# Optimization experiments

Measured on AMD Instinct MI355X. Metric: run time of the kernel, lower is better.

## Reference

```python
import jax, jax.numpy as jnp
import numpy as np

B, S, WIDTH, H = 4, 1024, 1024, 16
DH = WIDTH // H
NEG = -1000000000.0


def setup_inputs() -> dict:
    key = jax.random.key(0)
    ks = jax.random.split(key, 11)
    sc = 0.02
    return {
        "inp": jax.random.normal(ks[0], (B, S, WIDTH), dtype=jnp.float32),
        "mask": jax.random.randint(ks[1], (B, 1, S, S), 0, 2, dtype=jnp.int32),
        "wq": jax.random.normal(ks[2], (WIDTH, WIDTH), dtype=jnp.float32) * sc,
        "bq": jax.random.normal(ks[3], (WIDTH,), dtype=jnp.float32) * sc,
        "wk": jax.random.normal(ks[4], (WIDTH, WIDTH), dtype=jnp.float32) * sc,
        "bk": jax.random.normal(ks[5], (WIDTH,), dtype=jnp.float32) * sc,
        "wv": jax.random.normal(ks[6], (WIDTH, WIDTH), dtype=jnp.float32) * sc,
        "bv": jax.random.normal(ks[7], (WIDTH,), dtype=jnp.float32) * sc,
        "wo": jax.random.normal(ks[8], (WIDTH, WIDTH), dtype=jnp.float32) * sc,
        "bo": jax.random.normal(ks[9], (WIDTH,), dtype=jnp.float32) * sc,
    }


def reference(inp, mask, wq, bq, wk, bk, wv, bv, wo, bo):
    # torch Linear: y = x @ W.T + b
    q = inp @ wq.T + bq  # [B,S,WIDTH]
    k = inp @ wk.T + bk
    v = inp @ wv.T + bv
    # split heads -> [B,H,S,DH]
    q = q.reshape(B, S, H, DH).transpose(0, 2, 1, 3)
    k = k.reshape(B, S, H, DH).transpose(0, 2, 1, 3)
    v = v.reshape(B, S, H, DH).transpose(0, 2, 1, 3)
    scale = 1.0 / jnp.sqrt(jnp.float32(DH))
    qk = jnp.einsum("bhqd,bhkd->bhqk", q, k) * scale  # [B,H,S,S]
    qk = jnp.where(mask == 0, jnp.float32(NEG), qk)
    # NOTE: faithful to source, softmax over dim=1 (the HEAD axis), not keys
    attn = jax.nn.softmax(qk, axis=1)
    x = jnp.einsum("bhqk,bhkd->bhqd", attn, v)  # [B,H,S,DH]
    x = x.transpose(0, 2, 1, 3).reshape(B, S, WIDTH)
    return x @ wo.T + bo
```

## Files before the change

### kernel.cpp

```cpp
#include <hip/hip_runtime.h>


typedef float f32x4 __attribute__((ext_vector_type(4)));
typedef __bf16 bf16x8 __attribute__((ext_vector_type(8)));

__device__ __forceinline__ unsigned short f2bf(float f){
  unsigned int u = __builtin_bit_cast(unsigned int, f);
  u = (u + 0x7FFFu + ((u >> 16) & 1u)) >> 16;
  return (unsigned short)u;
}

__device__ __forceinline__ void gl16(const unsigned short* g, unsigned short* l){
  __builtin_amdgcn_global_load_lds(
      (const __attribute__((address_space(1))) void*)g,
      (__attribute__((address_space(3))) void*)l, 16, 0, 0);
}

__global__ __launch_bounds__(256) void cvt_kernel(const float* __restrict__ s,
                                                  unsigned short* __restrict__ d, int n4){
  int i = blockIdx.x * 256 + threadIdx.x;
  if (i < n4){
    float4 v = ((const float4*)s)[i];
    ushort4 o;
    o.x = f2bf(v.x); o.y = f2bf(v.y); o.z = f2bf(v.z); o.w = f2bf(v.w);
    ((ushort4*)d)[i] = o;
  }
}

__global__ __launch_bounds__(256) void cvt4_kernel(
    const float* __restrict__ s0, const float* __restrict__ s1,
    const float* __restrict__ s2, const float* __restrict__ s3,
    unsigned short* __restrict__ d0, unsigned short* __restrict__ d1,
    unsigned short* __restrict__ d2, unsigned short* __restrict__ d3){
  int i = blockIdx.x * 256 + threadIdx.x;
  int seg = i >> 18, j = i & 262143;
  const float* s = (seg == 0) ? s0 : (seg == 1) ? s1 : (seg == 2) ? s2 : s3;
  unsigned short* d = (seg == 0) ? d0 : (seg == 1) ? d1 : (seg == 2) ? d2 : d3;
  float4 v = ((const float4*)s)[j];
  ushort4 o;
  o.x = f2bf(v.x); o.y = f2bf(v.y); o.z = f2bf(v.z); o.w = f2bf(v.w);
  ((ushort4*)d)[j] = o;
}

template<int MODE>
__global__ __launch_bounds__(256) void gemm_bt(
    const unsigned short* __restrict__ A, const unsigned short* __restrict__ Wt,
    int M, int N, int K,
    float* __restrict__ outp,
    unsigned short* __restrict__ qws, unsigned short* __restrict__ kws,
    unsigned short* __restrict__ vws,
    const float* __restrict__ bias0, const float* __restrict__ bias1,
    const float* __restrict__ bias2)
{
  __shared__ unsigned short As_[128*32];
  __shared__ unsigned short Bs_[128*32];
  const int tid = threadIdx.x;
  const int lane = tid & 63;
  const int wid = tid >> 6;
  const int wr = wid >> 1, wc = wid & 1;
  const int m0 = blockIdx.x * 128, n0 = blockIdx.y * 128;
  const int lq = lane & 15, lg = lane >> 4;
  const int srow = (wid << 5) + (lane >> 2);
  const int scol = (lane & 3) << 3;
  const unsigned short* Ag = A  + (size_t)(m0 + srow)*K + scol;
  const unsigned short* Bg = Wt + (size_t)(n0 + srow)*K + scol;
  char* a_l0 = (char*)As_ + (wid << 11);
  char* b_l0 = (char*)Bs_ + (wid << 11);
  f32x4 acc[4][4] = {};

  for (int k0 = 0; k0 < K; k0 += 32){
    gl16(Ag + k0,                 (unsigned short*)a_l0);
    gl16(Ag + (size_t)16*K + k0,  (unsigned short*)(a_l0 + 1024));
    gl16(Bg + k0,                 (unsigned short*)b_l0);
    gl16(Bg + (size_t)16*K + k0,  (unsigned short*)(b_l0 + 1024));
    __syncthreads();
    bf16x8 af[4], wf[4];
    #pragma unroll
    for (int i = 0; i < 4; ++i){
      af[i] = *(const bf16x8*)((char*)As_ + ((((wr<<6)+(i<<4)+lq)) << 6) + (lg << 4));
      wf[i] = *(const bf16x8*)((char*)Bs_ + ((((wc<<6)+(i<<4)+lq)) << 6) + (lg << 4));
    }
    #pragma unroll
    for (int i = 0; i < 4; ++i)
      #pragma unroll
      for (int j = 0; j < 4; ++j)
        acc[i][j] = __builtin_amdgcn_mfma_f32_16x16x32_bf16(af[i], wf[j], acc[i][j], 0, 0, 0);
    __syncthreads();
  }

  if (MODE == 0){
    #pragma unroll
    for (int j = 0; j < 4; ++j){
      int ncol = n0 + wc*64 + j*16 + lq;
      float bv = bias0[ncol];
      #pragma unroll
      for (int i = 0; i < 4; ++i){
        int mrow = m0 + wr*64 + i*16 + lg*4;
        #pragma unroll
        for (int r = 0; r < 4; ++r)
          outp[(size_t)(mrow + r)*N + ncol] = acc[i][j][r] + bv;
      }
    }
  } else {
    const int sel = n0 >> 10;
    const float* bp = (sel == 0) ? bias0 : ((sel == 1) ? bias1 : bias2);
    #pragma unroll
    for (int j = 0; j < 4; ++j){
      int n  = n0 + wc*64 + j*16 + lq;
      int n1 = n & 1023;
      int h = n1 >> 6, d = n1 & 63;
      float bv = bp[n1];
      #pragma unroll
      for (int i = 0; i < 4; ++i){
        int mbase = m0 + wr*64 + i*16 + lg*4;
        #pragma unroll
        for (int r = 0; r < 4; ++r){
          int m = mbase + r;
          int b = m >> 10, s = m & 1023;
          unsigned short o = f2bf(acc[i][j][r] + bv);
          if (sel == 0)      qws[(size_t)((((b<<4) + h)<<10) + s)*64 + d] = o;
          else if (sel == 1) kws[(size_t)((((b<<4) + h)<<10) + s)*64 + d] = o;
          else               vws[(size_t)((((b<<4) + h)<<6) + d)*1024 + s] = o;
        }
      }
    }
  }
}

__global__ __launch_bounds__(512, 4) void qksm_kernel(
    const unsigned short* __restrict__ qws, const unsigned short* __restrict__ kws,
    const int* __restrict__ mask, unsigned short* __restrict__ pws, int qbase)
{
  __shared__ unsigned short Qs[16*16*64];
  const int tid = threadIdx.x;
  const int lane = tid & 63, w = tid >> 6;
  const int kt = blockIdx.x, qt = blockIdx.y, b = blockIdx.z;
  const int q0 = qbase + (qt << 4);
  const int lq = lane & 15, lg = lane >> 4;
  const int aswz = (lq & 7) << 4;

  for (int c = tid; c < 2048; c += 512){
    int e = c << 3;
    int h = e >> 10, q = (e >> 6) & 15, d0 = e & 63;
    uint4 v = *(const uint4*)(qws + (size_t)((((b<<4) + h)<<10) + q0 + q)*64 + d0);
    int byteoff = (((h<<10) + (q<<6) + d0) << 1) ^ ((q & 7) << 4);
    *(uint4*)((char*)Qs + byteoff) = v;
  }
  __syncthreads();

  const float kscale = 0.125f * 1.44269504f;
  for (int it = 0; it < 2; ++it){
    const int kb = (kt << 8) + (it << 7) + (w << 4);
    const int klocal = (it << 7) + (w << 4) + lq;
    f32x4 sc[16];
    #pragma unroll
    for (int h = 0; h < 16; ++h){
      int abase = (h << 11) + (lq << 7) + (lg << 4);
      bf16x8 a0 = *(const bf16x8*)((const char*)Qs + ((abase     ) ^ aswz));
      bf16x8 a1 = *(const bf16x8*)((const char*)Qs + ((abase + 64) ^ aswz));
      const unsigned short* kp = kws + (size_t)((((b<<4) + h)<<10) + kb + lq)*64 + (lg<<3);
      bf16x8 kf0 = *(const bf16x8*)(kp);
      bf16x8 kf1 = *(const bf16x8*)(kp + 32);
      f32x4 s = {};
      s = __builtin_amdgcn_mfma_f32_16x16x32_bf16(a0, kf0, s, 0, 0, 0);
      s = __builtin_amdgcn_mfma_f32_16x16x32_bf16(a1, kf1, s, 0, 0, 0);
      sc[h] = s;
    }
    const int* mp = mask + (size_t)((b<<10) + q0 + (lg<<2))*1024 + kb + lq;
    #pragma unroll
    for (int r = 0; r < 4; ++r){
      const int mv = mp[r << 10];
      float mx = sc[0][r];
      #pragma unroll
      for (int h = 1; h < 16; ++h) mx = fmaxf(mx, sc[h][r]);
      float e[16]; float sum = 0.f;
      #pragma unroll
      for (int h = 0; h < 16; ++h){
        e[h] = __builtin_amdgcn_exp2f((sc[h][r] - mx) * kscale);
        sum += e[h];
      }
      const float rs = __builtin_amdgcn_rcpf(sum);
      const int qloc = (qt << 4) + (lg << 2) + r;
      unsigned short* pp = pws + (b << 23) + (kt << 17) + (qloc << 8) + klocal;
      #pragma unroll
      for (int h = 0; h < 16; ++h){
        float pv = mv ? (e[h] * rs) : 0.0625f;
        pp[h << 19] = f2bf(pv);
      }
    }
  }
}

__global__ __launch_bounds__(256) void pv_kernel(
    const unsigned short* __restrict__ pws, const unsigned short* __restrict__ vws,
    unsigned short* __restrict__ xbf, int qbase)
{
  __shared__ unsigned short Ps_[128*32];
  __shared__ unsigned short Vs_[64*32];
  const int tid = threadIdx.x;
  const int lane = tid & 63;
  const int wid = tid >> 6;
  const int qt = blockIdx.x, bh = blockIdx.y;
  const int b = bh >> 4, h = bh & 15;
  const int lq = lane & 15, lg = lane >> 4;
  const int arow = (wid << 5) + (lane >> 2);
  const int scol = (lane & 3) << 3;
  const unsigned short* Ag = pws + ((size_t)bh << 19) + (((qt << 7) + arow) << 8) + scol;
  const int brow = (wid << 4) + (lane >> 2);
  const unsigned short* Bg = vws + ((size_t)bh << 16) + brow*1024 + scol;
  char* a_l0 = (char*)Ps_ + (wid << 11);
  char* b_l0 = (char*)Vs_ + (wid << 10);
  f32x4 acc[2][4] = {};

  for (int k0 = 0; k0 < 1024; k0 += 32){
    const int koff = ((k0 >> 8) << 17) + (k0 & 255);
    gl16(Ag + koff,              (unsigned short*)a_l0);
    gl16(Ag + koff + (16 << 8),  (unsigned short*)(a_l0 + 1024));
    gl16(Bg + k0,                (unsigned short*)b_l0);
    __syncthreads();
    bf16x8 af[2], wf[4];
    #pragma unroll
    for (int i = 0; i < 2; ++i)
      af[i] = *(const bf16x8*)((char*)Ps_ + ((((wid<<5)+(i<<4)+lq)) << 6) + (lg << 4));
    #pragma unroll
    for (int j = 0; j < 4; ++j)
      wf[j] = *(const bf16x8*)((char*)Vs_ + ((((j<<4)+lq)) << 6) + (lg << 4));
    #pragma unroll
    for (int i = 0; i < 2; ++i)
      #pragma unroll
      for (int j = 0; j < 4; ++j)
        acc[i][j] = __builtin_amdgcn_mfma_f32_16x16x32_bf16(af[i], wf[j], acc[i][j], 0, 0, 0);
    __syncthreads();
  }

  #pragma unroll
  for (int j = 0; j < 4; ++j){
    int d = (j << 4) + lq;
    #pragma unroll
    for (int i = 0; i < 2; ++i){
      #pragma unroll
      for (int r = 0; r < 4; ++r){
        int qrow = qbase + (qt << 7) + (wid << 5) + (i << 4) + (lg << 2) + r;
        xbf[(size_t)((b << 10) + qrow)*1024 + (h << 6) + d] = f2bf(acc[i][j][r]);
      }
    }
  }
}

extern "C" void kernel_launch(void* const* d_in, const int* in_sizes, int n_in,
                              void* d_out, int out_size, void* d_ws, size_t ws_size,
                              hipStream_t stream) {
  const float* inp = (const float*)d_in[0];
  const int*  mask = (const int*)d_in[1];
  const float* wq = (const float*)d_in[2];
  const float* bq = (const float*)d_in[3];
  const float* wk = (const float*)d_in[4];
  const float* bk = (const float*)d_in[5];
  const float* wv = (const float*)d_in[6];
  const float* bv = (const float*)d_in[7];
  const float* wo = (const float*)d_in[8];
  const float* bo = (const float*)d_in[9];
  float* out = (float*)d_out;

  char* ws = (char*)d_ws;
  unsigned short* inp_bf = (unsigned short*)(ws);
  unsigned short* wqkv   = (unsigned short*)(ws + (8u  << 20));
  unsigned short* wo_bf  = (unsigned short*)(ws + (14u << 20));
  unsigned short* qws    = (unsigned short*)(ws + (16u << 20));
  unsigned short* kws    = (unsigned short*)(ws + (24u << 20));
  unsigned short* vws    = (unsigned short*)(ws + (32u << 20));
  unsigned short* xbf    = (unsigned short*)(ws + (40u << 20));
  unsigned short* pws    = (unsigned short*)(ws + (48u << 20));

  cvt_kernel<<<4096, 256, 0, stream>>>(inp, inp_bf, 1048576);
  cvt4_kernel<<<4096, 256, 0, stream>>>(wq, wk, wv, wo,
                                        wqkv, wqkv + (1u << 20), wqkv + (2u << 20), wo_bf);

  gemm_bt<1><<<dim3(32, 24), 256, 0, stream>>>(inp_bf, wqkv, 4096, 3072, 1024,
                                               nullptr, qws, kws, vws, bq, bk, bv);

  for (int half = 0; half < 2; ++half){
    qksm_kernel<<<dim3(4, 32, 4), 512, 0, stream>>>(qws, kws, mask, pws, half * 512);
    pv_kernel<<<dim3(4, 64), 256, 0, stream>>>(pws, vws, xbf, half * 512);
  }

  gemm_bt<0><<<dim3(32, 8), 256, 0, stream>>>(xbf, wo_bf, 4096, 1024, 1024,
                                              out, nullptr, nullptr, nullptr, bo, nullptr, nullptr);
}
```

Baseline: 381.6 us.

## Stage softmax probabilities in LDS for coalesced row-major P stores

The QK-softmax kernel now writes its probabilities to a swizzled LDS tile and then copies them to global memory as 16-byte vector stores. This replaces the old scattered 2-byte stores with a plain row-major [b,h,q,k] layout, and the PV kernel's addressing is updated to match. Q is no longer staged in LDS but read straight from global per head. The change aims to cut uncoalesced write traffic, at the cost of two extra barriers per iteration and more global reads of Q.

```diff
diff --git a/kernel.cpp b/kernel.cpp
--- a/kernel.cpp
+++ b/kernel.cpp
@@ -131,34 +131,24 @@
     const unsigned short* __restrict__ qws, const unsigned short* __restrict__ kws,
     const int* __restrict__ mask, unsigned short* __restrict__ pws, int qbase)
 {
-  __shared__ unsigned short Qs[16*16*64];
+  __shared__ unsigned short Ps[32768];
   const int tid = threadIdx.x;
   const int lane = tid & 63, w = tid >> 6;
   const int kt = blockIdx.x, qt = blockIdx.y, b = blockIdx.z;
   const int q0 = qbase + (qt << 4);
   const int lq = lane & 15, lg = lane >> 4;
-  const int aswz = (lq & 7) << 4;
-
-  for (int c = tid; c < 2048; c += 512){
-    int e = c << 3;
-    int h = e >> 10, q = (e >> 6) & 15, d0 = e & 63;
-    uint4 v = *(const uint4*)(qws + (size_t)((((b<<4) + h)<<10) + q0 + q)*64 + d0);
-    int byteoff = (((h<<10) + (q<<6) + d0) << 1) ^ ((q & 7) << 4);
-    *(uint4*)((char*)Qs + byteoff) = v;
-  }
-  __syncthreads();
-
+  const int buf = w >> 2, ksub = w & 3;
   const float kscale = 0.125f * 1.44269504f;
+
   for (int it = 0; it < 2; ++it){
     const int kb = (kt << 8) + (it << 7) + (w << 4);
-    const int klocal = (it << 7) + (w << 4) + lq;
     f32x4 sc[16];
     #pragma unroll
     for (int h = 0; h < 16; ++h){
-      int abase = (h << 11) + (lq << 7) + (lg << 4);
-      bf16x8 a0 = *(const bf16x8*)((const char*)Qs + ((abase     ) ^ aswz));
-      bf16x8 a1 = *(const bf16x8*)((const char*)Qs + ((abase + 64) ^ aswz));
-      const unsigned short* kp = kws + (size_t)((((b<<4) + h)<<10) + kb + lq)*64 + (lg<<3);
+      const unsigned short* qp = qws + (size_t)((((b<<4)+h)<<10) + q0 + lq)*64 + (lg<<3);
+      bf16x8 a0 = *(const bf16x8*)(qp);
+      bf16x8 a1 = *(const bf16x8*)(qp + 32);
+      const unsigned short* kp = kws + (size_t)((((b<<4)+h)<<10) + kb + lq)*64 + (lg<<3);
       bf16x8 kf0 = *(const bf16x8*)(kp);
       bf16x8 kf1 = *(const bf16x8*)(kp + 32);
       f32x4 s = {};
@@ -180,14 +170,27 @@
         sum += e[h];
       }
       const float rs = __builtin_amdgcn_rcpf(sum);
-      const int qloc = (qt << 4) + (lg << 2) + r;
-      unsigned short* pp = pws + (b << 23) + (kt << 17) + (qloc << 8) + klocal;
+      const int q = (lg << 2) + r;
+      const int base = (buf << 15) | (q << 7) | (((ksub << 4) | lq) << 1);
+      const int swz = lg << 5;
       #pragma unroll
       for (int h = 0; h < 16; ++h){
         float pv = mv ? (e[h] * rs) : 0.0625f;
-        pp[h << 19] = f2bf(pv);
-      }
-    }
+        *(unsigned short*)((char*)Ps + ((base | (h << 11)) ^ swz)) = f2bf(pv);
+      }
+    }
+    __syncthreads();
+    #pragma unroll
+    for (int j = 0; j < 8; ++j){
+      int e = ((j << 9) + tid) << 3;
+      int bufr = e >> 14, h = (e >> 10) & 15, q = (e >> 6) & 15, k64 = e & 63;
+      int lbyte = (e << 1) ^ (((q >> 2) & 3) << 5);
+      uint4 v = *(const uint4*)((const char*)Ps + lbyte);
+      size_t go = ((size_t)b << 23) + ((size_t)h << 19) + ((size_t)((qt << 4) | q) << 10)
+                + (kt << 8) + (it << 7) + (bufr << 6) + k64;
+      *(uint4*)(pws + go) = v;
+    }
+    __syncthreads();
   }
 }
 
@@ -205,7 +208,7 @@
   const int lq = lane & 15, lg = lane >> 4;
   const int arow = (wid << 5) + (lane >> 2);
   const int scol = (lane & 3) << 3;
-  const unsigned short* Ag = pws + ((size_t)bh << 19) + (((qt << 7) + arow) << 8) + scol;
+  const unsigned short* Ag = pws + ((size_t)bh << 19) + ((size_t)((qt << 7) + arow) << 10) + scol;
   const int brow = (wid << 4) + (lane >> 2);
   const unsigned short* Bg = vws + ((size_t)bh << 16) + brow*1024 + scol;
   char* a_l0 = (char*)Ps_ + (wid << 11);
@@ -213,10 +216,9 @@
   f32x4 acc[2][4] = {};
 
   for (int k0 = 0; k0 < 1024; k0 += 32){
-    const int koff = ((k0 >> 8) << 17) + (k0 & 255);
-    gl16(Ag + koff,              (unsigned short*)a_l0);
-    gl16(Ag + koff + (16 << 8),  (unsigned short*)(a_l0 + 1024));
-    gl16(Bg + k0,                (unsigned short*)b_l0);
+    gl16(Ag + k0,             (unsigned short*)a_l0);
+    gl16(Ag + k0 + (16 << 10),(unsigned short*)(a_l0 + 1024));
+    gl16(Bg + k0,             (unsigned short*)b_l0);
     __syncthreads();
     bf16x8 af[2], wf[4];
     #pragma unroll
```

Measured after the change: 539.4 us. +41.4%, slower.
